# Kernel tuning notes

Hardware: AMD Instinct MI355X
Metric: run time of the kernel (lower is better)

Reference implementation:

```python
import jax, jax.numpy as jnp
import numpy as np

GAMMA = 0.96875  # RetNet decay, 1 - 2**-5


def setup_inputs() -> dict:
    key = jax.random.key(0)
    kq, kk, kv = jax.random.split(key, 3)
    B, T, D = 8, 4096, 64
    q = jax.random.normal(kq, (B, T, D), dtype=jnp.float32)
    k = jax.random.normal(kk, (B, T, D), dtype=jnp.float32)
    v = jax.random.normal(kv, (B, T, D), dtype=jnp.float32)
    return {"q": q, "k": k, "v": v}


def reference(q, k, v):
    # Parallel retention: out = (QK^T * D_gamma / sqrt(d)) V,
    # D_gamma[i,j] = gamma^(i-j) for i>=j else 0.
    B, T, D = q.shape
    dtype = q.dtype
    idx = jnp.arange(T)
    diff = idx[:, None] - idx[None, :]           # [T,T]
    gamma = jnp.asarray(GAMMA, dtype)
    decay = jnp.where(
        diff >= 0,
        gamma ** jnp.maximum(diff, 0).astype(dtype),
        jnp.zeros((), dtype),
    )                                            # [T,T] causal decay mask
    qk = jnp.einsum('btd,bsd->bts', q, k)        # [B,T,T]
    scale = jnp.asarray(np.sqrt(D), dtype)
    attn = qk * decay[None, :, :] / scale        # [B,T,T]
    out = jnp.einsum('bts,bsd->btd', attn, v)    # [B,T,D]
    return out
```

## Files before the change

### kernel.cpp

```cpp
#include <hip/hip_runtime.h>


using bf16x8 = __attribute__((ext_vector_type(8))) short;
using bf16x4 = __attribute__((ext_vector_type(4))) short;
using f32x4  = __attribute__((ext_vector_type(4))) float;

#define T_SEQ  4096
#define DHEAD  64
#define BM     64
#define BN     64
#define LDSS   72
#define NBACK  3

__device__ __forceinline__ short f2bf(float f) {
  union { float fv; unsigned u; } un; un.fv = f;
  unsigned r = un.u + 0x7FFFu + ((un.u >> 16) & 1u);
  return (short)(r >> 16);
}

__global__ __launch_bounds__(256, 2)
void retention_fwd(const float* __restrict__ qg,
                   const float* __restrict__ kg,
                   const float* __restrict__ vg,
                   float* __restrict__ outg) {
  constexpr float L2G   = -0.04580368961312478f;
  constexpr float GAMMA = 0.96875f;
  constexpr float SCALE = 0.125f;

  __shared__ short lds_q [BM * LDSS];
  __shared__ short lds_k [2][BN * LDSS];
  __shared__ short lds_vt[2][DHEAD * LDSS];
  __shared__ short lds_p [4 * 16 * LDSS];

  const int tid  = threadIdx.x;
  const int lane = tid & 63;
  const int w    = tid >> 6;
  const int qt   = blockIdx.x & 63;
  const int b    = blockIdx.x >> 6;
  const int iq0  = qt * BM;
  const long base = (long)b * T_SEQ * DHEAD;

  const int ntiles = (qt < NBACK ? qt : NBACK) + 1;

  float4 kreg[4], vreg[4];

  const float4* kbase4 = reinterpret_cast<const float4*>(kg + base);
  const float4* vbase4 = reinterpret_cast<const float4*>(vg + base);

  auto load_kv = [&](int jk0) {
    const float4* ksrc = kbase4 + jk0 * (DHEAD / 4);
    const float4* vsrc = vbase4 + jk0 * (DHEAD / 4);
#pragma unroll
    for (int rep = 0; rep < 4; ++rep) {
      kreg[rep] = ksrc[tid + rep * 256];
      vreg[rep] = vsrc[tid + rep * 256];
    }
  };

  auto stage_kv = [&](int buf) {
#pragma unroll
    for (int rep = 0; rep < 4; ++rep) {
      int idx = tid + rep * 256;
      int row = idx >> 4;
      int c4  = idx & 15;
      bf16x4 s4;
      s4[0] = f2bf(kreg[rep].x); s4[1] = f2bf(kreg[rep].y);
      s4[2] = f2bf(kreg[rep].z); s4[3] = f2bf(kreg[rep].w);
      *reinterpret_cast<bf16x4*>(&lds_k[buf][row * LDSS + c4 * 4]) = s4;
      lds_vt[buf][(c4 * 4 + 0) * LDSS + row] = f2bf(vreg[rep].x);
      lds_vt[buf][(c4 * 4 + 1) * LDSS + row] = f2bf(vreg[rep].y);
      lds_vt[buf][(c4 * 4 + 2) * LDSS + row] = f2bf(vreg[rep].z);
      lds_vt[buf][(c4 * 4 + 3) * LDSS + row] = f2bf(vreg[rep].w);
    }
  };

  {
    const float4* qsrc = reinterpret_cast<const float4*>(qg + base + (long)iq0 * DHEAD);
    float4 qreg[4];
#pragma unroll
    for (int rep = 0; rep < 4; ++rep) qreg[rep] = qsrc[tid + rep * 256];
    load_kv(iq0);
#pragma unroll
    for (int rep = 0; rep < 4; ++rep) {
      int idx = tid + rep * 256;
      int row = idx >> 4;
      int c4  = idx & 15;
      bf16x4 s4;
      s4[0] = f2bf(qreg[rep].x); s4[1] = f2bf(qreg[rep].y);
      s4[2] = f2bf(qreg[rep].z); s4[3] = f2bf(qreg[rep].w);
      *reinterpret_cast<bf16x4*>(&lds_q[row * LDSS + c4 * 4]) = s4;
    }
    stage_kv(0);
  }
  __syncthreads();

  const int koff = (lane >> 4) * 8;
  bf16x8 qf0, qf1;
  {
    int row = w * 16 + (lane & 15);
    qf0 = *reinterpret_cast<const bf16x8*>(&lds_q[row * LDSS + koff]);
    qf1 = *reinterpret_cast<const bf16x8*>(&lds_q[row * LDSS + 32 + koff]);
  }

  f32x4 oacc[4];
#pragma unroll
  for (int dt = 0; dt < 4; ++dt) { oacc[dt][0]=0.f; oacc[dt][1]=0.f; oacc[dt][2]=0.f; oacc[dt][3]=0.f; }

  int cur = 0;
  for (int t = 0; t < ntiles; ++t) {
    const int delta = t * BN;
    const bool pf = (t + 1 < ntiles);
    if (pf) load_kv(iq0 - (t + 1) * BN);

    const int nj = lane & 15;
    const int mi = (lane >> 4) * 4;
#pragma unroll
    for (int nt = 0; nt < 4; ++nt) {
      int krow = nt * 16 + (lane & 15);
      bf16x8 kf0 = *reinterpret_cast<const bf16x8*>(&lds_k[cur][krow * LDSS + koff]);
      bf16x8 kf1 = *reinterpret_cast<const bf16x8*>(&lds_k[cur][krow * LDSS + 32 + koff]);
      f32x4 s; s[0]=0.f; s[1]=0.f; s[2]=0.f; s[3]=0.f;
      s = __builtin_amdgcn_mfma_f32_16x16x32_bf16(qf0, kf0, s, 0, 0, 0);
      s = __builtin_amdgcn_mfma_f32_16x16x32_bf16(qf1, kf1, s, 0, 0, 0);
      int ebase = delta + w * 16 + mi - nt * 16 - nj;
      float g = exp2f((float)ebase * L2G) * SCALE;
#pragma unroll
      for (int r = 0; r < 4; ++r) {
        float sc = ((ebase + r) >= 0) ? g : 0.0f;
        lds_p[(w * 16 + mi + r) * LDSS + nt * 16 + nj] = f2bf(s[r] * sc);
        g *= GAMMA;
      }
    }
    asm volatile("s_waitcnt lgkmcnt(0)" ::: "memory");

    {
      int prow = (w * 16 + (lane & 15)) * LDSS + koff;
      bf16x8 pf0 = *reinterpret_cast<const bf16x8*>(&lds_p[prow]);
      bf16x8 pf1 = *reinterpret_cast<const bf16x8*>(&lds_p[prow + 32]);
#pragma unroll
      for (int dt = 0; dt < 4; ++dt) {
        int vrow = (dt * 16 + (lane & 15)) * LDSS + koff;
        bf16x8 vf0 = *reinterpret_cast<const bf16x8*>(&lds_vt[cur][vrow]);
        bf16x8 vf1 = *reinterpret_cast<const bf16x8*>(&lds_vt[cur][vrow + 32]);
        oacc[dt] = __builtin_amdgcn_mfma_f32_16x16x32_bf16(pf0, vf0, oacc[dt], 0, 0, 0);
        oacc[dt] = __builtin_amdgcn_mfma_f32_16x16x32_bf16(pf1, vf1, oacc[dt], 0, 0, 0);
      }
    }

    if (pf) stage_kv(cur ^ 1);
    __syncthreads();
    cur ^= 1;
  }

#pragma unroll
  for (int dt = 0; dt < 4; ++dt) {
#pragma unroll
    for (int r = 0; r < 4; ++r) {
      int i = iq0 + w * 16 + (lane >> 4) * 4 + r;
      int d = dt * 16 + (lane & 15);
      outg[base + (long)i * DHEAD + d] = oacc[dt][r];
    }
  }
}

extern "C" void kernel_launch(void* const* d_in, const int* in_sizes, int n_in,
                              void* d_out, int out_size, void* d_ws, size_t ws_size,
                              hipStream_t stream) {
  const float* q = (const float*)d_in[0];
  const float* k = (const float*)d_in[1];
  const float* v = (const float*)d_in[2];
  float* out = (float*)d_out;
  int total_rows = in_sizes[0] / DHEAD;
  int nblocks = total_rows / BM;
  retention_fwd<<<dim3(nblocks), dim3(256), 0, stream>>>(q, k, v, out);
}
```

Baseline: 82.83 us.

## Single-buffer K/V in LDS with register-cached fragments and higher occupancy

Drops the double-buffered K and V^T LDS tiles in favour of one buffer. All K and V fragments for a tile are first read into registers, and a barrier lets the next tile be staged into the same buffer. The launch bound rises to three blocks per CU, the per-subtile exp2 is replaced by a running multiply by gamma^-16, and MFMA priority is raised around the PV product. This costs an extra barrier per tile and more VGPR pressure under a tighter register budget, which could cause spills.

```diff
diff --git a/kernel.cpp b/kernel.cpp
--- a/kernel.cpp
+++ b/kernel.cpp
@@ -18,18 +18,19 @@
   return (short)(r >> 16);
 }
 
-__global__ __launch_bounds__(256, 2)
+__global__ __launch_bounds__(256, 3)
 void retention_fwd(const float* __restrict__ qg,
                    const float* __restrict__ kg,
                    const float* __restrict__ vg,
                    float* __restrict__ outg) {
   constexpr float L2G   = -0.04580368961312478f;
   constexpr float GAMMA = 0.96875f;
+  constexpr float GI16  = 1.6619242819629204f;
   constexpr float SCALE = 0.125f;
 
   __shared__ short lds_q [BM * LDSS];
-  __shared__ short lds_k [2][BN * LDSS];
-  __shared__ short lds_vt[2][DHEAD * LDSS];
+  __shared__ short lds_k [BN * LDSS];
+  __shared__ short lds_vt[DHEAD * LDSS];
   __shared__ short lds_p [4 * 16 * LDSS];
 
   const int tid  = threadIdx.x;
@@ -43,7 +44,6 @@
   const int ntiles = (qt < NBACK ? qt : NBACK) + 1;
 
   float4 kreg[4], vreg[4];
-
   const float4* kbase4 = reinterpret_cast<const float4*>(kg + base);
   const float4* vbase4 = reinterpret_cast<const float4*>(vg + base);
 
@@ -57,7 +57,7 @@
     }
   };
 
-  auto stage_kv = [&](int buf) {
+  auto stage_kv = [&]() {
 #pragma unroll
     for (int rep = 0; rep < 4; ++rep) {
       int idx = tid + rep * 256;
@@ -66,11 +66,11 @@
       bf16x4 s4;
       s4[0] = f2bf(kreg[rep].x); s4[1] = f2bf(kreg[rep].y);
       s4[2] = f2bf(kreg[rep].z); s4[3] = f2bf(kreg[rep].w);
-      *reinterpret_cast<bf16x4*>(&lds_k[buf][row * LDSS + c4 * 4]) = s4;
-      lds_vt[buf][(c4 * 4 + 0) * LDSS + row] = f2bf(vreg[rep].x);
-      lds_vt[buf][(c4 * 4 + 1) * LDSS + row] = f2bf(vreg[rep].y);
-      lds_vt[buf][(c4 * 4 + 2) * LDSS + row] = f2bf(vreg[rep].z);
-      lds_vt[buf][(c4 * 4 + 3) * LDSS + row] = f2bf(vreg[rep].w);
+      *reinterpret_cast<bf16x4*>(&lds_k[row * LDSS + c4 * 4]) = s4;
+      lds_vt[(c4 * 4 + 0) * LDSS + row] = f2bf(vreg[rep].x);
+      lds_vt[(c4 * 4 + 1) * LDSS + row] = f2bf(vreg[rep].y);
+      lds_vt[(c4 * 4 + 2) * LDSS + row] = f2bf(vreg[rep].z);
+      lds_vt[(c4 * 4 + 3) * LDSS + row] = f2bf(vreg[rep].w);
     }
   };
 
@@ -90,14 +90,15 @@
       s4[2] = f2bf(qreg[rep].z); s4[3] = f2bf(qreg[rep].w);
       *reinterpret_cast<bf16x4*>(&lds_q[row * LDSS + c4 * 4]) = s4;
     }
-    stage_kv(0);
+    stage_kv();
   }
   __syncthreads();
 
   const int koff = (lane >> 4) * 8;
+  const int l15  = lane & 15;
   bf16x8 qf0, qf1;
   {
-    int row = w * 16 + (lane & 15);
+    int row = w * 16 + l15;
     qf0 = *reinterpret_cast<const bf16x8*>(&lds_q[row * LDSS + koff]);
     qf1 = *reinterpret_cast<const bf16x8*>(&lds_q[row * LDSS + 32 + koff]);
   }
@@ -106,50 +107,58 @@
 #pragma unroll
   for (int dt = 0; dt < 4; ++dt) { oacc[dt][0]=0.f; oacc[dt][1]=0.f; oacc[dt][2]=0.f; oacc[dt][3]=0.f; }
 
-  int cur = 0;
   for (int t = 0; t < ntiles; ++t) {
     const int delta = t * BN;
     const bool pf = (t + 1 < ntiles);
     if (pf) load_kv(iq0 - (t + 1) * BN);
 
-    const int nj = lane & 15;
-    const int mi = (lane >> 4) * 4;
+    bf16x8 kf[4][2], vf[4][2];
 #pragma unroll
     for (int nt = 0; nt < 4; ++nt) {
-      int krow = nt * 16 + (lane & 15);
-      bf16x8 kf0 = *reinterpret_cast<const bf16x8*>(&lds_k[cur][krow * LDSS + koff]);
-      bf16x8 kf1 = *reinterpret_cast<const bf16x8*>(&lds_k[cur][krow * LDSS + 32 + koff]);
+      int frow = (nt * 16 + l15) * LDSS + koff;
+      kf[nt][0] = *reinterpret_cast<const bf16x8*>(&lds_k[frow]);
+      kf[nt][1] = *reinterpret_cast<const bf16x8*>(&lds_k[frow + 32]);
+      vf[nt][0] = *reinterpret_cast<const bf16x8*>(&lds_vt[frow]);
+      vf[nt][1] = *reinterpret_cast<const bf16x8*>(&lds_vt[frow + 32]);
+    }
+    asm volatile("s_waitcnt lgkmcnt(0)" ::: "memory");
+    __syncthreads();
+
+    const int mi = (lane >> 4) * 4;
+    const int ebase0 = delta + w * 16 + mi - l15;
+    float gq = exp2f((float)ebase0 * L2G) * SCALE;
+#pragma unroll
+    for (int nt = 0; nt < 4; ++nt) {
       f32x4 s; s[0]=0.f; s[1]=0.f; s[2]=0.f; s[3]=0.f;
-      s = __builtin_amdgcn_mfma_f32_16x16x32_bf16(qf0, kf0, s, 0, 0, 0);
-      s = __builtin_amdgcn_mfma_f32_16x16x32_bf16(qf1, kf1, s, 0, 0, 0);
-      int ebase = delta + w * 16 + mi - nt * 16 - nj;
-      float g = exp2f((float)ebase * L2G) * SCALE;
+      s = __builtin_amdgcn_mfma_f32_16x16x32_bf16(qf0, kf[nt][0], s, 0, 0, 0);
+      s = __builtin_amdgcn_mfma_f32_16x16x32_bf16(qf1, kf[nt][1], s, 0, 0, 0);
+      const int ebase = ebase0 - nt * 16;
+      float g = gq;
 #pragma unroll
       for (int r = 0; r < 4; ++r) {
         float sc = ((ebase + r) >= 0) ? g : 0.0f;
-        lds_p[(w * 16 + mi + r) * LDSS + nt * 16 + nj] = f2bf(s[r] * sc);
+        lds_p[(w * 16 + mi + r) * LDSS + nt * 16 + l15] = f2bf(s[r] * sc);
         g *= GAMMA;
       }
+      gq *= GI16;
     }
     asm volatile("s_waitcnt lgkmcnt(0)" ::: "memory");
 
     {
-      int prow = (w * 16 + (lane & 15)) * LDSS + koff;
+      int prow = (w * 16 + l15) * LDSS + koff;
       bf16x8 pf0 = *reinterpret_cast<const bf16x8*>(&lds_p[prow]);
       bf16x8 pf1 = *reinterpret_cast<const bf16x8*>(&lds_p[prow + 32]);
+      __builtin_amdgcn_s_setprio(1);
 #pragma unroll
       for (int dt = 0; dt < 4; ++dt) {
-        int vrow = (dt * 16 + (lane & 15)) * LDSS + koff;
-        bf16x8 vf0 = *reinterpret_cast<const bf16x8*>(&lds_vt[cur][vrow]);
-        bf16x8 vf1 = *reinterpret_cast<const bf16x8*>(&lds_vt[cur][vrow + 32]);
-        oacc[dt] = __builtin_amdgcn_mfma_f32_16x16x32_bf16(pf0, vf0, oacc[dt], 0, 0, 0);
-        oacc[dt] = __builtin_amdgcn_mfma_f32_16x16x32_bf16(pf1, vf1, oacc[dt], 0, 0, 0);
+        oacc[dt] = __builtin_amdgcn_mfma_f32_16x16x32_bf16(pf0, vf[dt][0], oacc[dt], 0, 0, 0);
+        oacc[dt] = __builtin_amdgcn_mfma_f32_16x16x32_bf16(pf1, vf[dt][1], oacc[dt], 0, 0, 0);
       }
+      __builtin_amdgcn_s_setprio(0);
     }
 
-    if (pf) stage_kv(cur ^ 1);
+    if (pf) stage_kv();
     __syncthreads();
-    cur ^= 1;
   }
 
 #pragma unroll
@@ -157,7 +166,7 @@
 #pragma unroll
     for (int r = 0; r < 4; ++r) {
       int i = iq0 + w * 16 + (lane >> 4) * 4 + r;
-      int d = dt * 16 + (lane & 15);
+      int d = dt * 16 + l15;
       outg[base + (long)i * DHEAD + d] = oacc[dt][r];
     }
   }
```

Measured after the change: 84.61 us. +2.1%, slower.
